# Kernel optimization log

Hardware: AMD Instinct MI355X
Metric: run time of the kernel (lower is better)

The kernel has to match this reference:

```python
import jax, jax.numpy as jnp
from jax import lax
import numpy as np

N, M, P, K = 2, 16384, 5023, 4
C_PLANE, HP = 32, 256
OUT_DIM = 32


def _harmonic(x):
    # pytorch3d HarmonicEmbedding(n=4, logspace, omega_0=1, append_input=True)
    f = jnp.asarray([1.0, 2.0, 4.0, 8.0], x.dtype)
    e = (x[..., None] * f).reshape(x.shape[:-1] + (-1,))  # [..., 12]
    return jnp.concatenate([jnp.sin(e), jnp.cos(e), x], axis=-1)  # [..., 27]


def _grid_sample2d(img, grid):
    # img [C,H,W], grid [M,2] (x->W, y->H) in [-1,1]; bilinear, zero pad, align_corners=False
    C, H, W = img.shape
    x = (grid[:, 0] + 1.0) * (W / 2.0) - 0.5
    y = (grid[:, 1] + 1.0) * (H / 2.0) - 0.5
    x0 = jnp.floor(x); y0 = jnp.floor(y)
    x1 = x0 + 1.0; y1 = y0 + 1.0
    wx1 = x - x0; wx0 = 1.0 - wx1
    wy1 = y - y0; wy0 = 1.0 - wy1
    def gather(ix, iy):
        valid = ((ix >= 0) & (ix < W) & (iy >= 0) & (iy < H)).astype(img.dtype)
        ixc = jnp.clip(ix, 0, W - 1).astype(jnp.int32)
        iyc = jnp.clip(iy, 0, H - 1).astype(jnp.int32)
        return img[:, iyc, ixc] * valid[None, :]  # [C,M]
    out = (gather(x0, y0) * (wx0 * wy0) + gather(x1, y0) * (wx1 * wy0)
           + gather(x0, y1) * (wx0 * wy1) + gather(x1, y1) * (wx1 * wy1))
    return out.T  # [M,C]


def _forward(coordinates, directions, points_position, tex_tplanes, emb_table,
             pw1, pb1, pw2, pb2, fw1, fb1, fw2, fb2, fw3, fb3, dw, db, rw1, rb1, rw2, rb2):
    c = coordinates
    p = points_position
    # --- triplane sampling (EG3D projections (x,y),(x,z),(z,x)), mean over planes ---
    proj = jnp.stack([c[..., :2],
                      c[..., jnp.array([0, 2])],
                      c[..., jnp.array([2, 0])]], axis=1)  # [N,3,M,2]
    tex = jax.vmap(jax.vmap(_grid_sample2d))(tex_tplanes, proj).mean(axis=1)  # [N,M,32]
    # --- KNN (squared distances, ascending, as pytorch3d knn_points) ---
    d2 = (jnp.sum(c * c, -1)[:, :, None] + jnp.sum(p * p, -1)[:, None, :]
          - 2.0 * jnp.einsum('nmc,npc->nmp', c, p))  # [N,M,P]
    negd, idx = lax.top_k(-d2, K)
    dist = -negd  # [N,M,K]
    nn = jax.vmap(lambda pts, i: pts[i])(p, idx)  # [N,M,K,3]
    pf = emb_table[idx]  # [N,M,K,32]
    rel = c[:, :, None, :] - nn
    rel = rel / jnp.maximum(jnp.linalg.norm(rel, axis=-1, keepdims=True), 1e-12)
    h = jnp.concatenate([pf, _harmonic(rel)], axis=-1)  # [N,M,K,59]
    h = jax.nn.relu(h @ pw1 + pb1) @ pw2 + pb2  # [N,M,K,32]
    w = 1.0 / dist
    w = w / jnp.sum(w, axis=1, keepdims=True)  # dim=1 exactly as in source
    pts_feat = jnp.sum(h * w[..., None], axis=2)  # [N,M,32]
    # --- dense MLP stack ---
    feat = jnp.concatenate([tex, pts_feat], axis=-1)  # [N,M,64]
    feat = jax.nn.relu(feat @ fw1 + fb1)
    feat = jax.nn.relu(feat @ fw2 + fb2)
    feat = feat @ fw3 + fb3  # [N,M,128]
    selector = jnp.all((c > -1.0) & (c < 1.0), axis=-1)  # [N,M]
    raw = (jax.nn.softplus(10.0 * (feat @ dw + db)) / 10.0) * selector[..., None]
    densities = 1.0 - jnp.exp(-raw)
    rays = directions / jnp.maximum(jnp.linalg.norm(directions, axis=-1, keepdims=True), 1e-12)
    rgb = jnp.concatenate([feat, _harmonic(rays)], axis=-1)  # [N,M,155]
    rgb = jax.nn.relu(rgb @ rw1 + rb1) @ rw2 + rb2  # [N,M,OUT_DIM]
    rgb = jnp.concatenate([jax.nn.sigmoid(rgb[..., :3]) * (1.0 + 2 * 0.001) - 0.001,
                           rgb[..., 3:]], axis=-1)
    return densities, rgb, dist


def setup_inputs() -> dict:
    key = jax.random.key(0)
    ks = jax.random.split(key, 16)
    rn = lambda k, s, sc=1.0: jax.random.normal(k, s, jnp.float32) * sc
    def lin(k, i, o):
        k1, k2 = jax.random.split(k)
        return rn(k1, (i, o), 1.0 / np.sqrt(i)), rn(k2, (o,), 0.01)
    coordinates = jax.random.uniform(ks[0], (N, M, 3), jnp.float32)
    directions = rn(ks[1], (N, M, 3))
    points_position = jax.random.uniform(ks[2], (N, P, 3), jnp.float32)
    tex_tplanes = rn(ks[3], (N, 3, C_PLANE, HP, HP))
    emb_table = rn(ks[4], (P, 32), 0.02)
    pw1, pb1 = lin(ks[5], 32 + 27, 64)
    pw2, pb2 = lin(ks[6], 64, 32)
    fw1, fb1 = lin(ks[7], 64, 128)
    fw2, fb2 = lin(ks[8], 128, 128)
    fw3, fb3 = lin(ks[9], 128, 128)
    dw, db = lin(ks[10], 128, 1)
    rw1, rb1 = lin(ks[11], 128 + 27, 64)
    rw2, rb2 = lin(ks[12], 64, OUT_DIM)
    return dict(coordinates=coordinates, directions=directions, points_position=points_position,
                tex_tplanes=tex_tplanes, emb_table=emb_table, pw1=pw1, pb1=pb1, pw2=pw2, pb2=pb2,
                fw1=fw1, fb1=fb1, fw2=fw2, fb2=fb2, fw3=fw3, fb3=fb3, dw=dw, db=db,
                rw1=rw1, rb1=rb1, rw2=rw2, rb2=rb2)


def reference(coordinates, directions, points_position, tex_tplanes, emb_table,
              pw1, pb1, pw2, pb2, fw1, fb1, fw2, fb2, fw3, fb3, dw, db, rw1, rb1, rw2, rb2):
    return _forward(coordinates, directions, points_position, tex_tplanes, emb_table,
                    pw1, pb1, pw2, pb2, fw1, fb1, fw2, fb2, fw3, fb3, dw, db, rw1, rb1, rw2, rb2)
```

## Files before the change

kernel.cpp:

```cpp
#include <hip/hip_runtime.h>
#include <float.h>
#include <math.h>

#define NB 2
#define MQ 16384
#define NQ (NB*MQ)
#define PP 5023
#define KNN 4
#define HPX 256
#define HWSZ (HPX*HPX)
#define GD 12
#define GC (GD*GD*GD)
#define CAND_MAX 1024

#define OUT_RGB_OFF  ((size_t)NQ)
#define OUT_DIST_OFF ((size_t)NQ + (size_t)NQ*32)

#define WS_SUMS_OFF   ((size_t)0x80000)
#define WS_PCNT_OFF   ((size_t)0x81000)
#define WS_PSTART_OFF ((size_t)0x85000)
#define WS_PCUR_OFF   ((size_t)0x89000)
#define WS_QCNT_OFF   ((size_t)0x8D000)
#define WS_QSTART_OFF ((size_t)0x91000)
#define WS_QCUR_OFF   ((size_t)0x95000)
#define WS_QID_OFF    ((size_t)0x99000)
#define WS_PG_OFF     ((size_t)0xC0000)
#define WS_PID_OFF    ((size_t)0xF0000)
#define WS_WP_OFF     ((size_t)0x100000)
#define WS_TEX_OFF    ((size_t)0x120000)

#define WP_PW1 0
#define WP_PW2 1920
#define WP_FW1 2944
#define WP_FW2 7040
#define WP_FW3 15232
#define WP_DW  23424
#define WP_RW1 23488
#define WP_RW2 28480

typedef __attribute__((ext_vector_type(2))) _Float16 half2v;

static __device__ __forceinline__ unsigned int pk2(float a, float b) {
    half2v h; h[0] = (_Float16)a; h[1] = (_Float16)b;
    return __builtin_bit_cast(unsigned int, h);
}
static __device__ __forceinline__ float2 upk(unsigned int u) {
    half2v h = __builtin_bit_cast(half2v, u);
    return make_float2((float)h[0], (float)h[1]);
}
static __device__ __forceinline__ float dot2(unsigned int a, unsigned int b, float c) {
    return __builtin_amdgcn_fdot2(__builtin_bit_cast(half2v, a),
                                  __builtin_bit_cast(half2v, b), c, false);
}
static __device__ __forceinline__ int cell_of(float x) {
    int g = (int)(x * (float)GD);
    return (g < 0) ? 0 : ((g > GD-1) ? GD-1 : g);
}

struct PackArgs {
    const float* src[8];
    int off[8]; int din[8]; int dout[8];
};
__global__ __launch_bounds__(256) void k_pack(PackArgs a, unsigned int* wp) {
    const int mid = blockIdx.y;
    const int idx = blockIdx.x * 256 + threadIdx.x;
    const int DIN = a.din[mid], DOUT = a.dout[mid];
    const int din2 = (DIN + 1) >> 1;
    if (idx >= din2 * DOUT) return;
    const int i2 = idx / DOUT, j = idx - i2 * DOUT;
    const float* s = a.src[mid];
    const float lo = s[(2*i2) * DOUT + j];
    const float hi = (2*i2 + 1 < DIN) ? s[(2*i2 + 1) * DOUT + j] : 0.f;
    wp[a.off[mid] + idx] = pk2(lo, hi);
}

__global__ __launch_bounds__(256) void k_transpose(const float* __restrict__ src,
                                                   unsigned int* __restrict__ dst) {
    const int tid = threadIdx.x;
    const int b = blockIdx.x;
    const int n3 = b >> 8;
    const int hw = ((b & 255) << 8) + tid;
    const float* s = src + (size_t)n3 * 32 * HWSZ + hw;
    float v[32];
#pragma unroll
    for (int c = 0; c < 32; ++c) v[c] = s[(size_t)c * HWSZ];
    uint4* d = (uint4*)(dst + ((size_t)n3 * HWSZ + hw) * 16);
#pragma unroll
    for (int c = 0; c < 4; ++c)
        d[c] = make_uint4(pk2(v[8*c], v[8*c+1]), pk2(v[8*c+2], v[8*c+3]),
                          pk2(v[8*c+4], v[8*c+5]), pk2(v[8*c+6], v[8*c+7]));
}

__global__ __launch_bounds__(256) void k_count(const float* __restrict__ pts,
                                               const float* __restrict__ coords,
                                               unsigned int* __restrict__ pcnt,
                                               unsigned int* __restrict__ qcnt) {
    const int i = blockIdx.x * 256 + threadIdx.x;
    if (i < NB * PP) {
        const int n = (i >= PP) ? 1 : 0;
        const float px = pts[3*i], py = pts[3*i+1], pz = pts[3*i+2];
        const int c = (cell_of(pz)*GD + cell_of(py))*GD + cell_of(px);
        atomicAdd(&pcnt[n*GC + c], 1u);
    } else if (i - NB*PP < NQ) {
        const int q = i - NB*PP;
        const int n = q >> 14;
        const float cx = coords[3*q], cy = coords[3*q+1], cz = coords[3*q+2];
        const int c = (cell_of(cz)*GD + cell_of(cy))*GD + cell_of(cx);
        atomicAdd(&qcnt[n*GC + c], 1u);
    }
}

__global__ __launch_bounds__(1024) void k_scan2(const unsigned int* __restrict__ pcnt,
                                                unsigned int* __restrict__ psta,
                                                unsigned int* __restrict__ pcur,
                                                const unsigned int* __restrict__ qcnt,
                                                unsigned int* __restrict__ qsta,
                                                unsigned int* __restrict__ qcur) {
    __shared__ unsigned int sc[1024];
    const int t = threadIdx.x;
#pragma unroll 1
    for (int which = 0; which < 2; ++which) {
        const unsigned int* cnt = which ? qcnt : pcnt;
        unsigned int* start  = which ? qsta : psta;
        unsigned int* cursor = which ? qcur : pcur;
        const int stride = which ? MQ : PP;
#pragma unroll 1
        for (int n = 0; n < 2; ++n) {
            const unsigned int* c = cnt + n*GC;
            unsigned int a = (2*t   < GC) ? c[2*t]   : 0u;
            unsigned int b = (2*t+1 < GC) ? c[2*t+1] : 0u;
            unsigned int s = a + b;
            sc[t] = s;
            __syncthreads();
            for (int off = 1; off < 1024; off <<= 1) {
                unsigned int v = (t >= off) ? sc[t - off] : 0u;
                __syncthreads();
                sc[t] += v;
                __syncthreads();
            }
            unsigned int excl = sc[t] - s;
            unsigned int base = n * stride;
            if (2*t < GC)   { start[n*GC + 2*t]   = base + excl;
                              cursor[n*GC + 2*t]  = base + excl; }
            if (2*t+1 < GC) { start[n*GC + 2*t+1] = base + excl + a;
                              cursor[n*GC + 2*t+1]= base + excl + a; }
            __syncthreads();
        }
    }
}

__global__ __launch_bounds__(256) void k_scatter(const float* __restrict__ pts,
                                                 const float* __restrict__ coords,
                                                 unsigned int* __restrict__ pcur,
                                                 unsigned int* __restrict__ qcur,
                                                 float4* __restrict__ pg,
                                                 int* __restrict__ pid,
                                                 int* __restrict__ qid) {
    const int i = blockIdx.x * 256 + threadIdx.x;
    if (i < NB * PP) {
        const int n = (i >= PP) ? 1 : 0;
        const int local = i - n * PP;
        const float px = pts[3*i], py = pts[3*i+1], pz = pts[3*i+2];
        const int c = (cell_of(pz)*GD + cell_of(py))*GD + cell_of(px);
        const unsigned int pos = atomicAdd(&pcur[n*GC + c], 1u);
        pg[pos] = make_float4(px, py, pz, fmaf(px, px, fmaf(py, py, pz*pz)));
        pid[pos] = local;
    } else if (i - NB*PP < NQ) {
        const int q = i - NB*PP;
        const int n = q >> 14;
        const float cx = coords[3*q], cy = coords[3*q+1], cz = coords[3*q+2];
        const int c = (cell_of(cz)*GD + cell_of(cy))*GD + cell_of(cx);
        const unsigned int pos = atomicAdd(&qcur[n*GC + c], 1u);
        qid[pos] = q;
    }
}

__global__ __launch_bounds__(256) void k_knn_cell(
    const float* __restrict__ coords,
    const unsigned int* __restrict__ pstart, const unsigned int* __restrict__ pcnt,
    const float4* __restrict__ pg, const int* __restrict__ pid,
    const unsigned int* __restrict__ qstart, const unsigned int* __restrict__ qcnt,
    const int* __restrict__ qid,
    float* __restrict__ odist, int* __restrict__ oidx)
{
    __shared__ float4 cand[CAND_MAX];
    __shared__ int    cidx[CAND_MAX];
    __shared__ unsigned int rs[25], ro[26];
    const int tid = threadIdx.x;
    const int bid = blockIdx.x;
    const int n = bid / GC, c = bid % GC;
    const unsigned int qn = qcnt[n*GC + c];
    if (qn == 0) return;
    const int gz = c / (GD*GD), gy = (c / GD) % GD, gx = c % GD;

    const int x0 = max(gx-2,0), x1 = min(gx+2,GD-1);
    const int y0 = max(gy-2,0), y1 = min(gy+2,GD-1), ny = y1-y0+1;
    const int z0 = max(gz-2,0), z1 = min(gz+2,GD-1), nz = z1-z0+1;
    const int nrow = ny*nz;

    __shared__ unsigned int rcnt[25];
    if (tid < nrow) {
        const int yy = y0 + tid % ny;
        const int zz = z0 + tid / ny;
        const int c0 = n*GC + (zz*GD + yy)*GD + x0;
        const int c1 = n*GC + (zz*GD + yy)*GD + x1;
        const unsigned int s = pstart[c0];
        rs[tid]   = s;
        rcnt[tid] = (pstart[c1] + pcnt[c1]) - s;
    }
    __syncthreads();
    if (tid == 0) {
        unsigned int acc = 0; ro[0] = 0;
        for (int t = 0; t < nrow; ++t) { acc += rcnt[t]; ro[t+1] = acc; }
    }
    __syncthreads();
    const unsigned int total = ro[nrow];
    const bool ovf = (total > CAND_MAX);
    if (!ovf) {
        for (unsigned int i = tid; i < total; i += 256) {
            int lo = 0, hi = nrow;
            while (hi - lo > 1) { int mid = (lo + hi) >> 1; if (ro[mid] <= i) lo = mid; else hi = mid; }
            const unsigned int src = rs[lo] + (i - ro[lo]);
            cand[i] = pg[src];
            cidx[i] = pid[src];
        }
    }
    __syncthreads();

    const float w = 1.0f / (float)GD;
    const float thresh = 4.f * w * w * 0.999f;
    const int grp = tid >> 4, l16 = tid & 15;
    const unsigned int qs = qstart[n*GC + c];

#define INS4(d, i) { \
        bool L3 = ((d) < bd3) || ((d) == bd3 && (i) < bi3); \
        bool L2 = ((d) < bd2) || ((d) == bd2 && (i) < bi2); \
        bool L1 = ((d) < bd1) || ((d) == bd1 && (i) < bi1); \
        bool L0 = ((d) < bd0) || ((d) == bd0 && (i) < bi0); \
        bd3 = L3 ? (L2 ? bd2 : (d)) : bd3;  bi3 = L3 ? (L2 ? bi2 : (i)) : bi3; \
        bd2 = L2 ? (L1 ? bd1 : (d)) : bd2;  bi2 = L2 ? (L1 ? bi1 : (i)) : bi2; \
        bd1 = L1 ? (L0 ? bd0 : (d)) : bd1;  bi1 = L1 ? (L0 ? bi0 : (i)) : bi1; \
        bd0 = L0 ? (d) : bd0;               bi0 = L0 ? (i) : bi0; }

#define MERGE16() { \
        float bd[4] = { bd0, bd1, bd2, bd3 }; \
        int   bi[4] = { bi0, bi1, bi2, bi3 }; \
        for (int mask = 1; mask < 16; mask <<= 1) { \
            float od[4]; int oi[4]; \
            for (int j = 0; j < 4; ++j) { od[j] = __shfl_xor(bd[j], mask); \
                                          oi[j] = __shfl_xor(bi[j], mask); } \
            float e[4]; int ei[4]; \
            for (int j = 0; j < 4; ++j) { \
                float ad = bd[j], xd = od[3-j]; \
                int   ai = bi[j], xi = oi[3-j]; \
                bool ta = (ad < xd) || (ad == xd && ai < xi); \
                e[j] = ta ? ad : xd; ei[j] = ta ? ai : xi; \
            } \
            { bool sw = (e[2] < e[0]) || (e[2] == e[0] && ei[2] < ei[0]); \
              if (sw) { float td=e[0]; e[0]=e[2]; e[2]=td; int ti=ei[0]; ei[0]=ei[2]; ei[2]=ti; } } \
            { bool sw = (e[3] < e[1]) || (e[3] == e[1] && ei[3] < ei[1]); \
              if (sw) { float td=e[1]; e[1]=e[3]; e[3]=td; int ti=ei[1]; ei[1]=ei[3]; ei[3]=ti; } } \
            { bool sw = (e[1] < e[0]) || (e[1] == e[0] && ei[1] < ei[0]); \
              if (sw) { float td=e[0]; e[0]=e[1]; e[1]=td; int ti=ei[0]; ei[0]=ei[1]; ei[1]=ti; } } \
            { bool sw = (e[3] < e[2]) || (e[3] == e[2] && ei[3] < ei[2]); \
              if (sw) { float td=e[2]; e[2]=e[3]; e[3]=td; int ti=ei[2]; ei[2]=ei[3]; ei[3]=ti; } } \
            for (int j = 0; j < 4; ++j) { bd[j] = e[j]; bi[j] = ei[j]; } \
        } \
        bd0 = bd[0]; bd1 = bd[1]; bd2 = bd[2]; bd3 = bd[3]; \
        bi0 = bi[0]; bi1 = bi[1]; bi2 = bi[2]; bi3 = bi[3]; }

#pragma unroll 1
    for (unsigned int qb = 0; qb < qn; qb += 16) {
        const unsigned int qi = qb + grp;
        if (qi >= qn) continue;
        const int q = qid[qs + qi];
        const float cx = coords[3*q], cy = coords[3*q+1], cz = coords[3*q+2];
        const float ccq = fmaf(cx, cx, fmaf(cy, cy, cz*cz));

        float bd0 = FLT_MAX, bd1 = FLT_MAX, bd2 = FLT_MAX, bd3 = FLT_MAX;
        int   bi0 = 0x7fffffff, bi1 = 0x7fffffff, bi2 = 0x7fffffff, bi3 = 0x7fffffff;

        if (!ovf) {
#pragma unroll 1
            for (unsigned int j = l16; j < total; j += 16) {
                const float4 P = cand[j];
                const int i = cidx[j];
                const float dt = fmaf(cx, P.x, fmaf(cy, P.y, cz * P.z));
                const float d = fmaf(-2.0f, dt, ccq + P.w);
                INS4(d, i)
            }
            MERGE16()
        }
        if (ovf || !(bd3 < thresh)) {
            bd0 = bd1 = bd2 = bd3 = FLT_MAX;
            bi0 = bi1 = bi2 = bi3 = 0x7fffffff;
#pragma unroll 1
            for (int j = l16; j < PP; j += 16) {
                const float4 P = pg[n*PP + j];
                const int i = pid[n*PP + j];
                const float dt = fmaf(cx, P.x, fmaf(cy, P.y, cz * P.z));
                const float d = fmaf(-2.0f, dt, ccq + P.w);
                INS4(d, i)
            }
            MERGE16()
        }
        if (l16 == 0) {
            *(float4*)(odist + (size_t)q*4) = make_float4(bd0, bd1, bd2, bd3);
            *(int4*)(oidx + (size_t)q*4)    = make_int4(bi0, bi1, bi2, bi3);
        }
    }
#undef INS4
#undef MERGE16
}

__global__ __launch_bounds__(1024) void k_sums(const float* __restrict__ dist,
                                               float* __restrict__ sums) {
    const int b = blockIdx.x;
    const int n = b >> 2, k = b & 3;
    float s = 0.f;
    for (int m = threadIdx.x; m < MQ; m += 1024)
        s += 1.0f / dist[((size_t)n * MQ + m) * 4 + k];
    __shared__ float red[1024];
    red[threadIdx.x] = s;
    __syncthreads();
    for (int off = 512; off > 0; off >>= 1) {
        if (threadIdx.x < off) red[threadIdx.x] += red[threadIdx.x + off];
        __syncthreads();
    }
    if (threadIdx.x == 0) sums[b] = red[0];
}

static __device__ __forceinline__ float harm_val(int h, float rx, float ry, float rz) {
    if (h >= 27) return 0.f;
    float v;
    if (h < 24) {
        int base = (h < 12) ? h : (h - 12);
        float rv = (base >> 2) == 0 ? rx : ((base >> 2) == 1 ? ry : rz);
        float e = rv * (float)(1 << (base & 3));
        v = (h < 12) ? sinf(e) : cosf(e);
    } else {
        v = (h == 24) ? rx : ((h == 25) ? ry : rz);
    }
    return v;
}

#define SW 128

template<int DIN2, int DOUT, int TILE>
__device__ __forceinline__ void gemv2(const unsigned int* Xp, int lane,
                                      const unsigned int* Wl,
                                      const float* __restrict__ bias, int j0,
                                      float (&aa)[TILE], float (&ab)[TILE]) {
    static_assert(TILE % 4 == 0, "");
#pragma unroll
    for (int u = 0; u < TILE; ++u) { aa[u] = bias[j0 + u]; ab[u] = aa[u]; }
#pragma unroll
    for (int i2 = 0; i2 < DIN2; ++i2) {
        const uint2 xv = *(const uint2*)(Xp + i2 * SW + 2*lane);
        const uint4* wr = (const uint4*)(Wl + i2 * DOUT + j0);
#pragma unroll
        for (int t = 0; t < TILE/4; ++t) {
            const uint4 w4 = wr[t];
            aa[4*t+0] = dot2(xv.x, w4.x, aa[4*t+0]);  ab[4*t+0] = dot2(xv.y, w4.x, ab[4*t+0]);
            aa[4*t+1] = dot2(xv.x, w4.y, aa[4*t+1]);  ab[4*t+1] = dot2(xv.y, w4.y, ab[4*t+1]);
            aa[4*t+2] = dot2(xv.x, w4.z, aa[4*t+2]);  ab[4*t+2] = dot2(xv.y, w4.z, ab[4*t+2]);
            aa[4*t+3] = dot2(xv.x, w4.w, aa[4*t+3]);  ab[4*t+3] = dot2(xv.y, w4.w, ab[4*t+3]);
        }
    }
}

__global__ __launch_bounds__(1024, 1) void k_main(
    const float* __restrict__ coords, const float* __restrict__ dirs,
    const float* __restrict__ pts, const float* __restrict__ tex_raw,
    const unsigned int* __restrict__ tex16, const float* __restrict__ emb,
    const unsigned int* __restrict__ wp,
    const float* __restrict__ pb1, const float* __restrict__ pb2,
    const float* __restrict__ fb1, const float* __restrict__ fb2,
    const float* __restrict__ fb3, const float* __restrict__ db,
    const float* __restrict__ rb1, const float* __restrict__ rb2,
    const int* __restrict__ idxbuf, const float* __restrict__ distbuf,
    const float* __restrict__ sums, float* __restrict__ out, int use_tex_t)
{
    __shared__ unsigned int S[128 * SW];
    __shared__ __align__(16) unsigned int W[8192];
    const int tid  = threadIdx.x;
    const int lane = tid & 63;
    const int wv   = __builtin_amdgcn_readfirstlane(tid >> 6);
    const int q0   = blockIdx.x * 128;
    const int n    = q0 >> 14;
    const int qa   = q0 + 2*lane, qb = qa + 1;

#define STAGE(dstu4, srcoff, len) { \
        const uint4* s4_ = (const uint4*)(wp + (srcoff)); \
        for (int i_ = tid; i_ < (len)/4; i_ += 1024) ((uint4*)W)[(dstu4) + i_] = s4_[i_]; }

    unsigned int tex_pack[2];
    {
        const int g = wv;
#pragma unroll
        for (int s = 0; s < 2; ++s) {
            const int q = qa + s;
            const float cx = coords[q*3+0], cy = coords[q*3+1], cz = coords[q*3+2];
            float a0 = 0.f, a1 = 0.f;
#pragma unroll
            for (int pl = 0; pl < 3; ++pl) {
                float gx = (pl == 2) ? cz : cx;
                float gy = (pl == 0) ? cy : ((pl == 1) ? cz : cx);
                float x = (gx + 1.f) * 128.f - 0.5f;
                float y = (gy + 1.f) * 128.f - 0.5f;
                float x0f = floorf(x), y0f = floorf(y);
                float wx1 = x - x0f, wy1 = y - y0f;
                float wx0 = 1.f - wx1, wy0 = 1.f - wy1;
                int x0 = (int)x0f, y0 = (int)y0f;
                int n3 = n * 3 + pl;
                int  xs[4] = { x0, x0+1, x0,   x0+1 };
                int  ys[4] = { y0, y0,   y0+1, y0+1 };
                float wt[4] = { wx0*wy0, wx1*wy0, wx0*wy1, wx1*wy1 };
#pragma unroll
                for (int c = 0; c < 4; ++c) {
                    int xi = xs[c], yi = ys[c];
                    if (xi >= 0 && xi < HPX && yi >= 0 && yi < HPX) {
                        float wgt = wt[c];
                        if (use_tex_t) {
                            const unsigned int v = tex16[
                                ((size_t)n3 * HWSZ + (size_t)yi * HPX + xi) * 16 + g];
                            const float2 f = upk(v);
                            a0 = fmaf(wgt, f.x, a0);
                            a1 = fmaf(wgt, f.y, a1);
                        } else {
                            size_t base = ((size_t)(n3 * 32 + g * 2)) * HWSZ + (size_t)yi * HPX + xi;
                            a0 = fmaf(wgt, tex_raw[base], a0);
                            a1 = fmaf(wgt, tex_raw[base + HWSZ], a1);
                        }
                    }
                }
            }
            tex_pack[s] = pk2(a0 * (1.f/3.f), a1 * (1.f/3.f));
        }
    }

    STAGE(0, WP_PW1, 1920)
    STAGE(512, WP_PW2, 1024)
    __syncthreads();

#pragma unroll 1
    for (int k = 0; k < KNN; ++k) {
        {
#pragma unroll
            for (int s = 0; s < 2; ++s) {
                const int q = qa + s;
                const int id = idxbuf[(size_t)q*4 + k];
                if (wv < 8) {
                    const float4 e = *(const float4*)(emb + (size_t)id * 32 + wv*4);
                    S[(64 + 2*wv    )*SW + 2*lane + s] = pk2(e.x, e.y);
                    S[(64 + 2*wv + 1)*SW + 2*lane + s] = pk2(e.z, e.w);
                } else {
                    const int w8 = wv - 8;
                    if (w8 < 7) {
                        const float cx = coords[q*3+0], cy = coords[q*3+1], cz = coords[q*3+2];
                        const float nx = pts[((size_t)n*PP + id)*3 + 0];
                        const float ny = pts[((size_t)n*PP + id)*3 + 1];
                        const float nz = pts[((size_t)n*PP + id)*3 + 2];
                        float rx = cx - nx, ry = cy - ny, rz = cz - nz;
                        float nrm = sqrtf(fmaf(rx, rx, fmaf(ry, ry, rz*rz)));
                        float inv = 1.f / fmaxf(nrm, 1e-12f);
                        rx *= inv; ry *= inv; rz *= inv;
#pragma unroll
                        for (int t = 0; t < 2; ++t) {
                            const int pr = 2*w8 + t;
                            S[(80 + pr)*SW + 2*lane + s] =
                                pk2(harm_val(2*pr, rx, ry, rz), harm_val(2*pr + 1, rx, ry, rz));
                        }
                    }
                }
            }
        }
        __syncthreads();
        {
            float aa[4], ab[4];
            gemv2<30, 64, 4>(S + 64*SW, lane, W, pb1, wv * 4, aa, ab);
            S[(96 + 2*wv    )*SW + 2*lane + 0] = pk2(fmaxf(aa[0], 0.f), fmaxf(aa[1], 0.f));
            S[(96 + 2*wv    )*SW + 2*lane + 1] = pk2(fmaxf(ab[0], 0.f), fmaxf(ab[1], 0.f));
            S[(96 + 2*wv + 1)*SW + 2*lane + 0] = pk2(fmaxf(aa[2], 0.f), fmaxf(aa[3], 0.f));
            S[(96 + 2*wv + 1)*SW + 2*lane + 1] = pk2(fmaxf(ab[2], 0.f), fmaxf(ab[3], 0.f));
        }
        __syncthreads();
        {
            float aa[2], ab[2];
            aa[0] = pb2[wv*2 + 0]; aa[1] = pb2[wv*2 + 1];
            ab[0] = aa[0]; ab[1] = aa[1];
#pragma unroll
            for (int i2 = 0; i2 < 32; ++i2) {
                const uint2 xv = *(const uint2*)(S + (96 + i2)*SW + 2*lane);
                const unsigned int w0 = W[2048 + i2*32 + wv*2 + 0];
                const unsigned int w1 = W[2048 + i2*32 + wv*2 + 1];
                aa[0] = dot2(xv.x, w0, aa[0]);  ab[0] = dot2(xv.y, w0, ab[0]);
                aa[1] = dot2(xv.x, w1, aa[1]);  ab[1] = dot2(xv.y, w1, ab[1]);
            }
            const float da = distbuf[(size_t)qa*4 + k];
            const float dbq = distbuf[(size_t)qb*4 + k];
            const float wka = (1.0f / da)  / sums[n*4 + k];
            const float wkb = (1.0f / dbq) / sums[n*4 + k];
            S[(k*16 + wv)*SW + 2*lane + 0] = pk2(wka * aa[0], wka * aa[1]);
            S[(k*16 + wv)*SW + 2*lane + 1] = pk2(wkb * ab[0], wkb * ab[1]);
        }
        __syncthreads();
    }

    {
        S[(64 + wv)*SW + 2*lane + 0] = tex_pack[0];
        S[(64 + wv)*SW + 2*lane + 1] = tex_pack[1];
#pragma unroll
        for (int s = 0; s < 2; ++s) {
            float a = 0.f, b = 0.f;
#pragma unroll
            for (int k = 0; k < 4; ++k) {
                float2 v = upk(S[(k*16 + wv)*SW + 2*lane + s]);
                a += v.x; b += v.y;
            }
            S[(80 + wv)*SW + 2*lane + s] = pk2(a, b);
        }
    }
    STAGE(0, WP_FW1, 4096)
    __syncthreads();
    {
        float aa[8], ab[8];
        gemv2<32, 128, 8>(S + 64*SW, lane, W, fb1, wv * 8, aa, ab);
#pragma unroll
        for (int u = 0; u < 4; ++u) {
            S[(4*wv + u)*SW + 2*lane + 0] = pk2(fmaxf(aa[2*u], 0.f), fmaxf(aa[2*u+1], 0.f));
            S[(4*wv + u)*SW + 2*lane + 1] = pk2(fmaxf(ab[2*u], 0.f), fmaxf(ab[2*u+1], 0.f));
        }
    }
    __syncthreads();
    STAGE(0, WP_FW2, 8192)
    __syncthreads();
    {
        float aa[8], ab[8];
        gemv2<64, 128, 8>(S, lane, W, fb2, wv * 8, aa, ab);
#pragma unroll
        for (int u = 0; u < 4; ++u) {
            S[(64 + 4*wv + u)*SW + 2*lane + 0] = pk2(fmaxf(aa[2*u], 0.f), fmaxf(aa[2*u+1], 0.f));
            S[(64 + 4*wv + u)*SW + 2*lane + 1] = pk2(fmaxf(ab[2*u], 0.f), fmaxf(ab[2*u+1], 0.f));
        }
    }
    __syncthreads();
    STAGE(0, WP_FW3, 8192)
    __syncthreads();
    {
        float aa[8], ab[8];
        gemv2<64, 128, 8>(S + 64*SW, lane, W, fb3, wv * 8, aa, ab);
#pragma unroll
        for (int u = 0; u < 4; ++u) {
            S[(4*wv + u)*SW + 2*lane + 0] = pk2(aa[2*u], aa[2*u+1]);
            S[(4*wv + u)*SW + 2*lane + 1] = pk2(ab[2*u], ab[2*u+1]);
        }
    }
    __syncthreads();
    STAGE(0, WP_RW1, 4992)
    STAGE(1248, WP_RW2, 1024)
    STAGE(1504, WP_DW, 64)
    if (wv < 14) {
#pragma unroll
        for (int s = 0; s < 2; ++s) {
            const int q = qa + s;
            float dx = dirs[q*3+0], dy = dirs[q*3+1], dz = dirs[q*3+2];
            float dn = sqrtf(fmaf(dx, dx, fmaf(dy, dy, dz*dz)));
            float inv = 1.f / fmaxf(dn, 1e-12f);
            dx *= inv; dy *= inv; dz *= inv;
            S[(64 + wv)*SW + 2*lane + s] = pk2(harm_val(2*wv, dx, dy, dz),
                                               harm_val(2*wv + 1, dx, dy, dz));
        }
    }
    __syncthreads();
    {
        float aa[4], ab[4];
        gemv2<78, 64, 4>(S, lane, W, rb1, wv * 4, aa, ab);
        S[(78 + 2*wv    )*SW + 2*lane + 0] = pk2(fmaxf(aa[0], 0.f), fmaxf(aa[1], 0.f));
        S[(78 + 2*wv    )*SW + 2*lane + 1] = pk2(fmaxf(ab[0], 0.f), fmaxf(ab[1], 0.f));
        S[(78 + 2*wv + 1)*SW + 2*lane + 0] = pk2(fmaxf(aa[2], 0.f), fmaxf(aa[3], 0.f));
        S[(78 + 2*wv + 1)*SW + 2*lane + 1] = pk2(fmaxf(ab[2], 0.f), fmaxf(ab[3], 0.f));
    }
    __syncthreads();
    {
        float aa[2], ab[2];
        aa[0] = rb2[wv*2 + 0]; aa[1] = rb2[wv*2 + 1];
        ab[0] = aa[0]; ab[1] = aa[1];
#pragma unroll
        for (int i2 = 0; i2 < 32; ++i2) {
            const uint2 xv = *(const uint2*)(S + (78 + i2)*SW + 2*lane);
            const unsigned int w0 = W[4992 + i2*32 + wv*2 + 0];
            const unsigned int w1 = W[4992 + i2*32 + wv*2 + 1];
            aa[0] = dot2(xv.x, w0, aa[0]);  ab[0] = dot2(xv.y, w0, ab[0]);
            aa[1] = dot2(xv.x, w1, aa[1]);  ab[1] = dot2(xv.y, w1, ab[1]);
        }
#pragma unroll
        for (int u = 0; u < 2; ++u) {
            const int j = wv*2 + u;
            float va = (u == 0) ? aa[0] : aa[1];
            float vb = (u == 0) ? ab[0] : ab[1];
            if (j < 3) {
                va = 1.002f * (1.f / (1.f + expf(-va))) - 0.001f;
                vb = 1.002f * (1.f / (1.f + expf(-vb))) - 0.001f;
            }
            out[OUT_RGB_OFF + (size_t)qa*32 + j] = va;
            out[OUT_RGB_OFF + (size_t)qb*32 + j] = vb;
        }
        if (wv == 15) {
            float za = db[0], zb = db[0];
#pragma unroll 1
            for (int i2 = 0; i2 < 64; ++i2) {
                const uint2 xv = *(const uint2*)(S + i2*SW + 2*lane);
                const unsigned int wz = W[6016 + i2];
                za = dot2(xv.x, wz, za);
                zb = dot2(xv.y, wz, zb);
            }
#pragma unroll
            for (int s = 0; s < 2; ++s) {
                const int q = qa + s;
                const float z = (s == 0) ? za : zb;
                const float cx = coords[q*3+0], cy = coords[q*3+1], cz = coords[q*3+2];
                float selv = (cx > -1.f && cx < 1.f && cy > -1.f && cy < 1.f &&
                              cz > -1.f && cz < 1.f) ? 1.f : 0.f;
                float t10 = 10.f * z;
                float sp = (t10 > 20.f) ? t10 : log1pf(expf(t10));
                float raw = sp * 0.1f * selv;
                out[q] = 1.f - expf(-raw);
            }
        }
    }
#undef STAGE
}

extern "C" void kernel_launch(void* const* d_in, const int* in_sizes, int n_in,
                              void* d_out, int out_size, void* d_ws, size_t ws_size,
                              hipStream_t stream) {
    (void)in_sizes; (void)n_in; (void)out_size;
    const float* coords = (const float*)d_in[0];
    const float* dirs   = (const float*)d_in[1];
    const float* pts    = (const float*)d_in[2];
    const float* tex    = (const float*)d_in[3];
    const float* emb    = (const float*)d_in[4];
    const float* pw1 = (const float*)d_in[5];  const float* pb1 = (const float*)d_in[6];
    const float* pw2 = (const float*)d_in[7];  const float* pb2 = (const float*)d_in[8];
    const float* fw1 = (const float*)d_in[9];  const float* fb1 = (const float*)d_in[10];
    const float* fw2 = (const float*)d_in[11]; const float* fb2 = (const float*)d_in[12];
    const float* fw3 = (const float*)d_in[13]; const float* fb3 = (const float*)d_in[14];
    const float* dw  = (const float*)d_in[15]; const float* db  = (const float*)d_in[16];
    const float* rw1 = (const float*)d_in[17]; const float* rb1 = (const float*)d_in[18];
    const float* rw2 = (const float*)d_in[19]; const float* rb2 = (const float*)d_in[20];

    float*        out     = (float*)d_out;
    int*          wsidx   = (int*)d_ws;
    float*        wssums  = (float*)((char*)d_ws + WS_SUMS_OFF);
    unsigned int* wspcnt  = (unsigned int*)((char*)d_ws + WS_PCNT_OFF);
    unsigned int* wspsta  = (unsigned int*)((char*)d_ws + WS_PSTART_OFF);
    unsigned int* wspcur  = (unsigned int*)((char*)d_ws + WS_PCUR_OFF);
    unsigned int* wsqcnt  = (unsigned int*)((char*)d_ws + WS_QCNT_OFF);
    unsigned int* wsqsta  = (unsigned int*)((char*)d_ws + WS_QSTART_OFF);
    unsigned int* wsqcur  = (unsigned int*)((char*)d_ws + WS_QCUR_OFF);
    int*          wsqid   = (int*)((char*)d_ws + WS_QID_OFF);
    float4*       wspg    = (float4*)((char*)d_ws + WS_PG_OFF);
    int*          wspid   = (int*)((char*)d_ws + WS_PID_OFF);
    unsigned int* wswp    = (unsigned int*)((char*)d_ws + WS_WP_OFF);
    unsigned int* wstex   = (unsigned int*)((char*)d_ws + WS_TEX_OFF);

    const size_t need_tex = WS_TEX_OFF + (size_t)6 * HWSZ * 16 * 4;
    const int use_t = (ws_size >= need_tex) ? 1 : 0;

    PackArgs pa;
    pa.src[0] = pw1; pa.off[0] = WP_PW1; pa.din[0] = 59;  pa.dout[0] = 64;
    pa.src[1] = pw2; pa.off[1] = WP_PW2; pa.din[1] = 64;  pa.dout[1] = 32;
    pa.src[2] = fw1; pa.off[2] = WP_FW1; pa.din[2] = 64;  pa.dout[2] = 128;
    pa.src[3] = fw2; pa.off[3] = WP_FW2; pa.din[3] = 128; pa.dout[3] = 128;
    pa.src[4] = fw3; pa.off[4] = WP_FW3; pa.din[4] = 128; pa.dout[4] = 128;
    pa.src[5] = dw;  pa.off[5] = WP_DW;  pa.din[5] = 128; pa.dout[5] = 1;
    pa.src[6] = rw1; pa.off[6] = WP_RW1; pa.din[6] = 155; pa.dout[6] = 64;
    pa.src[7] = rw2; pa.off[7] = WP_RW2; pa.din[7] = 64;  pa.dout[7] = 32;

    const int nitems = NB*PP + NQ;
    hipMemsetAsync((char*)d_ws + WS_PCNT_OFF, 0, WS_QSTART_OFF - WS_PCNT_OFF, stream);
    k_pack<<<dim3(32, 8), 256, 0, stream>>>(pa, wswp);
    if (use_t) k_transpose<<<6 * 256, 256, 0, stream>>>(tex, wstex);
    k_count<<<(nitems + 255)/256, 256, 0, stream>>>(pts, coords, wspcnt, wsqcnt);
    k_scan2<<<1, 1024, 0, stream>>>(wspcnt, wspsta, wspcur, wsqcnt, wsqsta, wsqcur);
    k_scatter<<<(nitems + 255)/256, 256, 0, stream>>>(pts, coords, wspcur, wsqcur,
                                                      wspg, wspid, wsqid);
    k_knn_cell<<<NB*GC, 256, 0, stream>>>(coords, wspsta, wspcnt, wspg, wspid,
                                          wsqsta, wsqcnt, wsqid,
                                          out + OUT_DIST_OFF, wsidx);
    k_sums<<<8, 1024, 0, stream>>>(out + OUT_DIST_OFF, wssums);
    k_main<<<NQ / 128, 1024, 0, stream>>>(coords, dirs, pts, tex, wstex, emb,
                                          wswp, pb1, pb2, fb1, fb2, fb3, db, rb1, rb2,
                                          wsidx, out + OUT_DIST_OFF, wssums, out, use_t);
}
```

Measured before the change: 280.2 us.

## Fuse setup kernels, fold inverse-distance sums into KNN, overlap gathers, stage RGB stores

Merges the weight pack, texture transpose and cell count kernels into a single launch. The inverse-distance sum kernel is dropped and its work done with float atomics inside the KNN kernel. The main kernel now prefetches the next neighbor's embedding and harmonic gather before the barrier, which removes one barrier per neighbor, and it stages RGB outputs in shared memory so they can be written as coalesced float4 stores. It also unrolls the density loop. Float atomic accumulation makes the sums order-dependent and adds contention on 8 addresses, and the extra shared buffer may reduce occupancy.

```diff
diff --git a/kernel.cpp b/kernel.cpp
--- a/kernel.cpp
+++ b/kernel.cpp
@@ -57,56 +57,58 @@
     return (g < 0) ? 0 : ((g > GD-1) ? GD-1 : g);
 }
 
-struct PackArgs {
+struct FusedArgs {
     const float* src[8];
     int off[8]; int din[8]; int dout[8];
 };
-__global__ __launch_bounds__(256) void k_pack(PackArgs a, unsigned int* wp) {
-    const int mid = blockIdx.y;
-    const int idx = blockIdx.x * 256 + threadIdx.x;
-    const int DIN = a.din[mid], DOUT = a.dout[mid];
-    const int din2 = (DIN + 1) >> 1;
-    if (idx >= din2 * DOUT) return;
-    const int i2 = idx / DOUT, j = idx - i2 * DOUT;
-    const float* s = a.src[mid];
-    const float lo = s[(2*i2) * DOUT + j];
-    const float hi = (2*i2 + 1 < DIN) ? s[(2*i2 + 1) * DOUT + j] : 0.f;
-    wp[a.off[mid] + idx] = pk2(lo, hi);
-}
-
-__global__ __launch_bounds__(256) void k_transpose(const float* __restrict__ src,
-                                                   unsigned int* __restrict__ dst) {
+__global__ __launch_bounds__(256) void k_fused(
+    FusedArgs a, unsigned int* __restrict__ wp,
+    const float* __restrict__ tex, unsigned int* __restrict__ tex16,
+    const float* __restrict__ pts, const float* __restrict__ coords,
+    unsigned int* __restrict__ pcnt, unsigned int* __restrict__ qcnt,
+    int use_t)
+{
+    const int b = blockIdx.x;
     const int tid = threadIdx.x;
-    const int b = blockIdx.x;
-    const int n3 = b >> 8;
-    const int hw = ((b & 255) << 8) + tid;
-    const float* s = src + (size_t)n3 * 32 * HWSZ + hw;
-    float v[32];
-#pragma unroll
-    for (int c = 0; c < 32; ++c) v[c] = s[(size_t)c * HWSZ];
-    uint4* d = (uint4*)(dst + ((size_t)n3 * HWSZ + hw) * 16);
-#pragma unroll
-    for (int c = 0; c < 4; ++c)
-        d[c] = make_uint4(pk2(v[8*c], v[8*c+1]), pk2(v[8*c+2], v[8*c+3]),
-                          pk2(v[8*c+4], v[8*c+5]), pk2(v[8*c+6], v[8*c+7]));
-}
-
-__global__ __launch_bounds__(256) void k_count(const float* __restrict__ pts,
-                                               const float* __restrict__ coords,
-                                               unsigned int* __restrict__ pcnt,
-                                               unsigned int* __restrict__ qcnt) {
-    const int i = blockIdx.x * 256 + threadIdx.x;
-    if (i < NB * PP) {
-        const int n = (i >= PP) ? 1 : 0;
-        const float px = pts[3*i], py = pts[3*i+1], pz = pts[3*i+2];
-        const int c = (cell_of(pz)*GD + cell_of(py))*GD + cell_of(px);
-        atomicAdd(&pcnt[n*GC + c], 1u);
-    } else if (i - NB*PP < NQ) {
-        const int q = i - NB*PP;
-        const int n = q >> 14;
-        const float cx = coords[3*q], cy = coords[3*q+1], cz = coords[3*q+2];
-        const int c = (cell_of(cz)*GD + cell_of(cy))*GD + cell_of(cx);
-        atomicAdd(&qcnt[n*GC + c], 1u);
+    if (b < 1536) {
+        if (!use_t) return;
+        const int n3 = b >> 8;
+        const int hw = ((b & 255) << 8) + tid;
+        const float* s = tex + (size_t)n3 * 32 * HWSZ + hw;
+        float v[32];
+#pragma unroll
+        for (int c = 0; c < 32; ++c) v[c] = s[(size_t)c * HWSZ];
+        uint4* d = (uint4*)(tex16 + ((size_t)n3 * HWSZ + hw) * 16);
+#pragma unroll
+        for (int c = 0; c < 4; ++c)
+            d[c] = make_uint4(pk2(v[8*c], v[8*c+1]), pk2(v[8*c+2], v[8*c+3]),
+                              pk2(v[8*c+4], v[8*c+5]), pk2(v[8*c+6], v[8*c+7]));
+    } else if (b < 1536 + 256) {
+        const int b2 = b - 1536;
+        const int mid = b2 >> 5;
+        const int idx = (b2 & 31) * 256 + tid;
+        const int DIN = a.din[mid], DOUT = a.dout[mid];
+        const int din2 = (DIN + 1) >> 1;
+        if (idx >= din2 * DOUT) return;
+        const int i2 = idx / DOUT, j = idx - i2 * DOUT;
+        const float* s = a.src[mid];
+        const float lo = s[(2*i2) * DOUT + j];
+        const float hi = (2*i2 + 1 < DIN) ? s[(2*i2 + 1) * DOUT + j] : 0.f;
+        wp[a.off[mid] + idx] = pk2(lo, hi);
+    } else {
+        const int i = (b - 1792) * 256 + tid;
+        if (i < NB * PP) {
+            const int n = (i >= PP) ? 1 : 0;
+            const float px = pts[3*i], py = pts[3*i+1], pz = pts[3*i+2];
+            const int c = (cell_of(pz)*GD + cell_of(py))*GD + cell_of(px);
+            atomicAdd(&pcnt[n*GC + c], 1u);
+        } else if (i - NB*PP < NQ) {
+            const int q = i - NB*PP;
+            const int n = q >> 14;
+            const float cx = coords[3*q], cy = coords[3*q+1], cz = coords[3*q+2];
+            const int c = (cell_of(cz)*GD + cell_of(cy))*GD + cell_of(cx);
+            atomicAdd(&qcnt[n*GC + c], 1u);
+        }
     }
 }
 
@@ -181,7 +183,8 @@
     const float4* __restrict__ pg, const int* __restrict__ pid,
     const unsigned int* __restrict__ qstart, const unsigned int* __restrict__ qcnt,
     const int* __restrict__ qid,
-    float* __restrict__ odist, int* __restrict__ oidx)
+    float* __restrict__ odist, int* __restrict__ oidx,
+    float* __restrict__ sums)
 {
     __shared__ float4 cand[CAND_MAX];
     __shared__ int    cidx[CAND_MAX];
@@ -307,27 +310,14 @@
         if (l16 == 0) {
             *(float4*)(odist + (size_t)q*4) = make_float4(bd0, bd1, bd2, bd3);
             *(int4*)(oidx + (size_t)q*4)    = make_int4(bi0, bi1, bi2, bi3);
+            atomicAdd(&sums[n*4 + 0], 1.0f / bd0);
+            atomicAdd(&sums[n*4 + 1], 1.0f / bd1);
+            atomicAdd(&sums[n*4 + 2], 1.0f / bd2);
+            atomicAdd(&sums[n*4 + 3], 1.0f / bd3);
         }
     }
 #undef INS4
 #undef MERGE16
-}
-
-__global__ __launch_bounds__(1024) void k_sums(const float* __restrict__ dist,
-                                               float* __restrict__ sums) {
-    const int b = blockIdx.x;
-    const int n = b >> 2, k = b & 3;
-    float s = 0.f;
-    for (int m = threadIdx.x; m < MQ; m += 1024)
-        s += 1.0f / dist[((size_t)n * MQ + m) * 4 + k];
-    __shared__ float red[1024];
-    red[threadIdx.x] = s;
-    __syncthreads();
-    for (int off = 512; off > 0; off >>= 1) {
-        if (threadIdx.x < off) red[threadIdx.x] += red[threadIdx.x + off];
-        __syncthreads();
-    }
-    if (threadIdx.x == 0) sums[b] = red[0];
 }
 
 static __device__ __forceinline__ float harm_val(int h, float rx, float ry, float rz) {
@@ -383,16 +373,48 @@
 {
     __shared__ unsigned int S[128 * SW];
     __shared__ __align__(16) unsigned int W[8192];
+    __shared__ float Rstg[128 * 33];
     const int tid  = threadIdx.x;
     const int lane = tid & 63;
     const int wv   = __builtin_amdgcn_readfirstlane(tid >> 6);
     const int q0   = blockIdx.x * 128;
     const int n    = q0 >> 14;
-    const int qa   = q0 + 2*lane, qb = qa + 1;
+    const int qa   = q0 + 2*lane;
 
 #define STAGE(dstu4, srcoff, len) { \
         const uint4* s4_ = (const uint4*)(wp + (srcoff)); \
         for (int i_ = tid; i_ < (len)/4; i_ += 1024) ((uint4*)W)[(dstu4) + i_] = s4_[i_]; }
+
+    auto gatherA = [&](int kk) {
+#pragma unroll
+        for (int s = 0; s < 2; ++s) {
+            const int q = qa + s;
+            const int id = idxbuf[(size_t)q*4 + kk];
+            if (wv < 8) {
+                const float4 e = *(const float4*)(emb + (size_t)id * 32 + wv*4);
+                S[(64 + 2*wv    )*SW + 2*lane + s] = pk2(e.x, e.y);
+                S[(64 + 2*wv + 1)*SW + 2*lane + s] = pk2(e.z, e.w);
+            } else {
+                const int w8 = wv - 8;
+                if (w8 < 7) {
+                    const float cx = coords[q*3+0], cy = coords[q*3+1], cz = coords[q*3+2];
+                    const float nx = pts[((size_t)n*PP + id)*3 + 0];
+                    const float ny = pts[((size_t)n*PP + id)*3 + 1];
+                    const float nz = pts[((size_t)n*PP + id)*3 + 2];
+                    float rx = cx - nx, ry = cy - ny, rz = cz - nz;
+                    float nrm = sqrtf(fmaf(rx, rx, fmaf(ry, ry, rz*rz)));
+                    float inv = 1.f / fmaxf(nrm, 1e-12f);
+                    rx *= inv; ry *= inv; rz *= inv;
+#pragma unroll
+                    for (int t = 0; t < 2; ++t) {
+                        const int pr = 2*w8 + t;
+                        S[(80 + pr)*SW + 2*lane + s] =
+                            pk2(harm_val(2*pr, rx, ry, rz), harm_val(2*pr + 1, rx, ry, rz));
+                    }
+                }
+            }
+        }
+    };
 
     unsigned int tex_pack[2];
     {
@@ -441,41 +463,11 @@
 
     STAGE(0, WP_PW1, 1920)
     STAGE(512, WP_PW2, 1024)
+    gatherA(0);
     __syncthreads();
 
 #pragma unroll 1
     for (int k = 0; k < KNN; ++k) {
-        {
-#pragma unroll
-            for (int s = 0; s < 2; ++s) {
-                const int q = qa + s;
-                const int id = idxbuf[(size_t)q*4 + k];
-                if (wv < 8) {
-                    const float4 e = *(const float4*)(emb + (size_t)id * 32 + wv*4);
-                    S[(64 + 2*wv    )*SW + 2*lane + s] = pk2(e.x, e.y);
-                    S[(64 + 2*wv + 1)*SW + 2*lane + s] = pk2(e.z, e.w);
-                } else {
-                    const int w8 = wv - 8;
-                    if (w8 < 7) {
-                        const float cx = coords[q*3+0], cy = coords[q*3+1], cz = coords[q*3+2];
-                        const float nx = pts[((size_t)n*PP + id)*3 + 0];
-                        const float ny = pts[((size_t)n*PP + id)*3 + 1];
-                        const float nz = pts[((size_t)n*PP + id)*3 + 2];
-                        float rx = cx - nx, ry = cy - ny, rz = cz - nz;
-                        float nrm = sqrtf(fmaf(rx, rx, fmaf(ry, ry, rz*rz)));
-                        float inv = 1.f / fmaxf(nrm, 1e-12f);
-                        rx *= inv; ry *= inv; rz *= inv;
-#pragma unroll
-                        for (int t = 0; t < 2; ++t) {
-                            const int pr = 2*w8 + t;
-                            S[(80 + pr)*SW + 2*lane + s] =
-                                pk2(harm_val(2*pr, rx, ry, rz), harm_val(2*pr + 1, rx, ry, rz));
-                        }
-                    }
-                }
-            }
-        }
-        __syncthreads();
         {
             float aa[4], ab[4];
             gemv2<30, 64, 4>(S + 64*SW, lane, W, pb1, wv * 4, aa, ab);
@@ -497,13 +489,14 @@
                 aa[0] = dot2(xv.x, w0, aa[0]);  ab[0] = dot2(xv.y, w0, ab[0]);
                 aa[1] = dot2(xv.x, w1, aa[1]);  ab[1] = dot2(xv.y, w1, ab[1]);
             }
-            const float da = distbuf[(size_t)qa*4 + k];
-            const float dbq = distbuf[(size_t)qb*4 + k];
+            const float da  = distbuf[(size_t)qa*4 + k];
+            const float dbq = distbuf[(size_t)(qa+1)*4 + k];
             const float wka = (1.0f / da)  / sums[n*4 + k];
             const float wkb = (1.0f / dbq) / sums[n*4 + k];
             S[(k*16 + wv)*SW + 2*lane + 0] = pk2(wka * aa[0], wka * aa[1]);
             S[(k*16 + wv)*SW + 2*lane + 1] = pk2(wkb * ab[0], wkb * ab[1]);
         }
+        if (k < KNN-1) gatherA(k+1);
         __syncthreads();
     }
 
@@ -603,12 +596,12 @@
                 va = 1.002f * (1.f / (1.f + expf(-va))) - 0.001f;
                 vb = 1.002f * (1.f / (1.f + expf(-vb))) - 0.001f;
             }
-            out[OUT_RGB_OFF + (size_t)qa*32 + j] = va;
-            out[OUT_RGB_OFF + (size_t)qb*32 + j] = vb;
+            Rstg[(2*lane    ) * 33 + j] = va;
+            Rstg[(2*lane + 1) * 33 + j] = vb;
         }
         if (wv == 15) {
             float za = db[0], zb = db[0];
-#pragma unroll 1
+#pragma unroll 8
             for (int i2 = 0; i2 < 64; ++i2) {
                 const uint2 xv = *(const uint2*)(S + i2*SW + 2*lane);
                 const unsigned int wz = W[6016 + i2];
@@ -628,6 +621,17 @@
                 out[q] = 1.f - expf(-raw);
             }
         }
+    }
+    __syncthreads();
+    {
+        const int cq = tid >> 3;
+        const int j0 = (tid & 7) * 4;
+        float4 v;
+        v.x = Rstg[cq*33 + j0 + 0];
+        v.y = Rstg[cq*33 + j0 + 1];
+        v.z = Rstg[cq*33 + j0 + 2];
+        v.w = Rstg[cq*33 + j0 + 3];
+        *(float4*)(out + OUT_RGB_OFF + ((size_t)(q0 + cq))*32 + j0) = v;
     }
 #undef STAGE
 }
@@ -668,28 +672,27 @@
     const size_t need_tex = WS_TEX_OFF + (size_t)6 * HWSZ * 16 * 4;
     const int use_t = (ws_size >= need_tex) ? 1 : 0;
 
-    PackArgs pa;
-    pa.src[0] = pw1; pa.off[0] = WP_PW1; pa.din[0] = 59;  pa.dout[0] = 64;
-    pa.src[1] = pw2; pa.off[1] = WP_PW2; pa.din[1] = 64;  pa.dout[1] = 32;
-    pa.src[2] = fw1; pa.off[2] = WP_FW1; pa.din[2] = 64;  pa.dout[2] = 128;
-    pa.src[3] = fw2; pa.off[3] = WP_FW2; pa.din[3] = 128; pa.dout[3] = 128;
-    pa.src[4] = fw3; pa.off[4] = WP_FW3; pa.din[4] = 128; pa.dout[4] = 128;
-    pa.src[5] = dw;  pa.off[5] = WP_DW;  pa.din[5] = 128; pa.dout[5] = 1;
-    pa.src[6] = rw1; pa.off[6] = WP_RW1; pa.din[6] = 155; pa.dout[6] = 64;
-    pa.src[7] = rw2; pa.off[7] = WP_RW2; pa.din[7] = 64;  pa.dout[7] = 32;
+    FusedArgs fa;
+    fa.src[0] = pw1; fa.off[0] = WP_PW1; fa.din[0] = 59;  fa.dout[0] = 64;
+    fa.src[1] = pw2; fa.off[1] = WP_PW2; fa.din[1] = 64;  fa.dout[1] = 32;
+    fa.src[2] = fw1; fa.off[2] = WP_FW1; fa.din[2] = 64;  fa.dout[2] = 128;
+    fa.src[3] = fw2; fa.off[3] = WP_FW2; fa.din[3] = 128; fa.dout[3] = 128;
+    fa.src[4] = fw3; fa.off[4] = WP_FW3; fa.din[4] = 128; fa.dout[4] = 128;
+    fa.src[5] = dw;  fa.off[5] = WP_DW;  fa.din[5] = 128; fa.dout[5] = 1;
+    fa.src[6] = rw1; fa.off[6] = WP_RW1; fa.din[6] = 155; fa.dout[6] = 64;
+    fa.src[7] = rw2; fa.off[7] = WP_RW2; fa.din[7] = 64;  fa.dout[7] = 32;
 
     const int nitems = NB*PP + NQ;
-    hipMemsetAsync((char*)d_ws + WS_PCNT_OFF, 0, WS_QSTART_OFF - WS_PCNT_OFF, stream);
-    k_pack<<<dim3(32, 8), 256, 0, stream>>>(pa, wswp);
-    if (use_t) k_transpose<<<6 * 256, 256, 0, stream>>>(tex, wstex);
-    k_count<<<(nitems + 255)/256, 256, 0, stream>>>(pts, coords, wspcnt, wsqcnt);
+    const int count_blocks = (nitems + 255) / 256;
+    hipMemsetAsync((char*)d_ws + WS_SUMS_OFF, 0, WS_QSTART_OFF - WS_SUMS_OFF, stream);
+    k_fused<<<1792 + count_blocks, 256, 0, stream>>>(fa, wswp, tex, wstex,
+                                                     pts, coords, wspcnt, wsqcnt, use_t);
     k_scan2<<<1, 1024, 0, stream>>>(wspcnt, wspsta, wspcur, wsqcnt, wsqsta, wsqcur);
-    k_scatter<<<(nitems + 255)/256, 256, 0, stream>>>(pts, coords, wspcur, wsqcur,
-                                                      wspg, wspid, wsqid);
+    k_scatter<<<count_blocks, 256, 0, stream>>>(pts, coords, wspcur, wsqcur,
+                                                wspg, wspid, wsqid);
     k_knn_cell<<<NB*GC, 256, 0, stream>>>(coords, wspsta, wspcnt, wspg, wspid,
                                           wsqsta, wsqcnt, wsqid,
-                                          out + OUT_DIST_OFF, wsidx);
-    k_sums<<<8, 1024, 0, stream>>>(out + OUT_DIST_OFF, wssums);
+                                          out + OUT_DIST_OFF, wsidx, wssums);
     k_main<<<NQ / 128, 1024, 0, stream>>>(coords, dirs, pts, tex, wstex, emb,
                                           wswp, pb1, pb2, fb1, fb2, fb3, db, rb1, rb2,
                                           wsidx, out + OUT_DIST_OFF, wssums, out, use_t);
```

After: 739.7 us. 2.64x slower.
